# Performance work log

Measured on AMD Instinct MI355X. Metric: run time of the kernel, lower is better.

The kernel has to match this reference:

```python
import jax, jax.numpy as jnp
import numpy as np

EPS = 1e-08


def setup_inputs() -> dict:
    key = jax.random.key(0)
    kx, ky = jax.random.split(key)
    x = jax.random.normal(kx, (8192, 512), dtype=jnp.float32)
    y = jax.random.normal(ky, (8192, 512), dtype=jnp.float32)
    return {"x": x, "y": y}


def reference(x, y):
    # Faithful to torch.nn.CosineSimilarity(dim=2, eps=EPS) applied to the
    # broadcast pair (x[i], y[j]):
    #   cos[i, j] = <x_i, y_j> / (max(||x_i||, eps) * max(||y_j||, eps))
    # Algebraically equivalent efficient form: normalize rows once, then GEMM.
    xn = x / jnp.maximum(jnp.linalg.norm(x, axis=1, keepdims=True), EPS)  # [Nx, L]
    yn = y / jnp.maximum(jnp.linalg.norm(y, axis=1, keepdims=True), EPS)  # [Ny, L]
    return jnp.einsum('il,jl->ij', xn, yn)  # [Nx, Ny]
```

## Files before the change

### kernel.cpp

```cpp
#include <hip/hip_runtime.h>


typedef __attribute__((ext_vector_type(8))) short bf16x8;
typedef __attribute__((ext_vector_type(4))) float f32x4;
typedef __attribute__((ext_vector_type(8))) unsigned short ushort8;

#define M_DIM 8192
#define N_DIM 8192
#define K_DIM 512

static __device__ __forceinline__ unsigned short f32_to_bf16(float f) {
  unsigned int u = __float_as_uint(f);
  u = (u + 0x7FFFu + ((u >> 16) & 1u)) >> 16;
  return (unsigned short)u;
}

__global__ __launch_bounds__(256) void normalize_rows(
    const float* __restrict__ x, const float* __restrict__ y,
    unsigned short* __restrict__ out) {
  const int wid = threadIdx.x >> 6;
  const int lane = threadIdx.x & 63;
  const int row = (blockIdx.x << 2) + wid;
  const float* src = row < M_DIM ? x + (size_t)row * K_DIM
                                 : y + (size_t)(row - M_DIM) * K_DIM;
  const float4* r = (const float4*)src;
  float4 v0 = r[lane * 2];
  float4 v1 = r[lane * 2 + 1];
  float ss = v0.x * v0.x + v0.y * v0.y + v0.z * v0.z + v0.w * v0.w +
             v1.x * v1.x + v1.y * v1.y + v1.z * v1.z + v1.w * v1.w;
#pragma unroll
  for (int off = 32; off; off >>= 1) ss += __shfl_xor(ss, off, 64);
  const float s = 1.0f / fmaxf(sqrtf(ss), 1e-8f);
  const float f[8] = {v0.x, v0.y, v0.z, v0.w, v1.x, v1.y, v1.z, v1.w};
  union { ushort8 v; unsigned short u[8]; } o;
#pragma unroll
  for (int i = 0; i < 8; ++i) o.u[i] = f32_to_bf16(f[i] * s);
  *(ushort8*)(out + (size_t)row * K_DIM + lane * 8) = o.v;
}

static __device__ __forceinline__ void gl16(const unsigned short* g, char* l) {
  __builtin_amdgcn_global_load_lds(
      (const __attribute__((address_space(1))) unsigned int*)g,
      (__attribute__((address_space(3))) unsigned int*)l, 16, 0, 0);
}

#define BAR() __builtin_amdgcn_s_barrier()
#define SBAR() __builtin_amdgcn_sched_barrier(0)
#define LGKM0() do { asm volatile("s_waitcnt lgkmcnt(0)" ::: "memory"); \
                     __builtin_amdgcn_sched_barrier(0); } while (0)
#define VMCNT(n) do { asm volatile("s_waitcnt vmcnt(" #n ")" ::: "memory"); \
                      __builtin_amdgcn_sched_barrier(0); } while (0)

__global__ __launch_bounds__(256, 3) void cosgemm(
    const unsigned short* __restrict__ A,
    const unsigned short* __restrict__ B,
    float* __restrict__ C) {
  extern __shared__ char smem[];

  const int tid = threadIdx.x;
  const int lane = tid & 63;
  const int wid = tid >> 6;
  const int wm = wid >> 1;
  const int wn = wid & 1;
  const int lr16 = lane & 15;
  const int hq = lane >> 4;
  const int sw = hq ^ (lr16 & 3);

  const int bid = blockIdx.x;
  const int idx = bid >> 3;
  const int by = ((bid & 7) << 3) + (idx & 7);
  const int bx = idx >> 3;
  const int row0 = by << 7;
  const int col0 = bx << 7;

  const int srl = lane >> 2;
  const int ssl = (lane & 3) ^ (srl & 3);
  const unsigned short* pA =
      A + (size_t)(row0 + (wid << 4) + srl) * K_DIM + ssl * 8;
  const unsigned short* pB =
      B + (size_t)(col0 + (wid << 4) + srl) * K_DIM + ssl * 8;

  auto stageA = [&](int buf, int h, int T) {
    char* l = smem + buf * 16384 + (h << 12) + (wid << 10);
    gl16(pA + T * 32 + (size_t)(h << 6) * K_DIM, l);
  };
  auto stageB = [&](int buf, int h, int T) {
    char* l = smem + buf * 16384 + 8192 + (h << 12) + (wid << 10);
    gl16(pB + T * 32 + (size_t)(h << 6) * K_DIM, l);
  };

  bf16x8 af[4], bf[4];
  f32x4 acc[4][4] = {};

  auto ldA = [&](int buf) {
#pragma unroll
    for (int m = 0; m < 4; ++m) {
      const int row = (wm << 6) + m * 16 + lr16;
      af[m] = *(const bf16x8*)(smem + buf * 16384 + row * 64 + (sw << 4));
    }
  };
  auto ldB = [&](int buf, int g) {
#pragma unroll
    for (int j = 0; j < 2; ++j) {
      const int row = (wn << 6) + (g * 2 + j) * 16 + lr16;
      bf[g * 2 + j] = *(const bf16x8*)(smem + buf * 16384 + 8192 + row * 64 +
                                       (sw << 4));
    }
  };
  auto mm = [&](int g) {
    __builtin_amdgcn_s_setprio(1);
#pragma unroll
    for (int m = 0; m < 4; ++m)
#pragma unroll
      for (int j = 0; j < 2; ++j)
        acc[m][g * 2 + j] = __builtin_amdgcn_mfma_f32_16x16x32_bf16(
            af[m], bf[g * 2 + j], acc[m][g * 2 + j], 0, 0, 0);
    __builtin_amdgcn_s_setprio(0);
  };

  stageA(0, 0, 0); stageA(0, 1, 0); stageB(0, 0, 0); stageB(0, 1, 0);
  stageA(1, 0, 1); stageA(1, 1, 1); stageB(1, 0, 1); stageB(1, 1, 1);
  VMCNT(4);
  BAR(); SBAR();

#pragma unroll 1
  for (int t = 0; t < 16; ++t) {
    const int cb = t % 3, nb = (t + 2) % 3;
    const bool st = (t < 14);
    ldA(cb); ldB(cb, 0);
    if (st) { stageA(nb, 0, t + 2); stageA(nb, 1, t + 2); }
    BAR(); LGKM0(); mm(0); BAR();
    ldB(cb, 1);
    if (st) { stageB(nb, 0, t + 2); stageB(nb, 1, t + 2); }
    BAR(); LGKM0(); mm(1);
    if (st) { VMCNT(4); } else { VMCNT(0); }
    BAR(); SBAR();
  }

  float* S = (float*)(smem + wid * 4352);
  const int crow0 = row0 + (wm << 6);
  const int ccol0 = col0 + (wn << 6);
#pragma unroll
  for (int fm = 0; fm < 4; ++fm) {
#pragma unroll
    for (int fn = 0; fn < 4; ++fn)
#pragma unroll
      for (int q = 0; q < 4; ++q)
        S[(hq * 4 + q) * 68 + fn * 16 + lr16] = acc[fm][fn][q];
#pragma unroll
    for (int r = 0; r < 4; ++r) {
      f32x4 v = *(const f32x4*)&S[(r * 4 + hq) * 68 + lr16 * 4];
      __builtin_nontemporal_store(
          v, (f32x4*)&C[(size_t)(crow0 + fm * 16 + r * 4 + hq) * N_DIM +
                        ccol0 + lr16 * 4]);
    }
  }
}

extern "C" void kernel_launch(void* const* d_in, const int* in_sizes, int n_in,
                              void* d_out, int out_size, void* d_ws, size_t ws_size,
                              hipStream_t stream) {
  const float* x = (const float*)d_in[0];
  const float* y = (const float*)d_in[1];
  float* out = (float*)d_out;
  unsigned short* xn = (unsigned short*)d_ws;
  unsigned short* yn = xn + (size_t)M_DIM * K_DIM;

  (void)hipFuncSetAttribute((const void*)cosgemm,
                            hipFuncAttributeMaxDynamicSharedMemorySize, 49152);

  normalize_rows<<<(M_DIM + N_DIM) / 4, 256, 0, stream>>>(x, y, xn);
  cosgemm<<<(M_DIM / 128) * (N_DIM / 128), 256, 49152, stream>>>(xn, yn, out);
}
```

Measured before the change: 111.1 us.

## Give each wave private LDS tiles and drop block barriers in GEMM loop

```diff
diff --git a/kernel.cpp b/kernel.cpp
--- a/kernel.cpp
+++ b/kernel.cpp
@@ -44,14 +44,13 @@
       (__attribute__((address_space(3))) unsigned int*)l, 16, 0, 0);
 }
 
-#define BAR() __builtin_amdgcn_s_barrier()
 #define SBAR() __builtin_amdgcn_sched_barrier(0)
 #define LGKM0() do { asm volatile("s_waitcnt lgkmcnt(0)" ::: "memory"); \
                      __builtin_amdgcn_sched_barrier(0); } while (0)
 #define VMCNT(n) do { asm volatile("s_waitcnt vmcnt(" #n ")" ::: "memory"); \
                       __builtin_amdgcn_sched_barrier(0); } while (0)
 
-__global__ __launch_bounds__(256, 3) void cosgemm(
+__global__ __launch_bounds__(256, 2) void cosgemm(
     const unsigned short* __restrict__ A,
     const unsigned short* __restrict__ B,
     float* __restrict__ C) {
@@ -70,76 +69,64 @@
   const int idx = bid >> 3;
   const int by = ((bid & 7) << 3) + (idx & 7);
   const int bx = idx >> 3;
-  const int row0 = by << 7;
-  const int col0 = bx << 7;
+  const int row0 = (by << 7) + (wm << 6);
+  const int col0 = (bx << 7) + (wn << 6);
 
   const int srl = lane >> 2;
   const int ssl = (lane & 3) ^ (srl & 3);
-  const unsigned short* pA =
-      A + (size_t)(row0 + (wid << 4) + srl) * K_DIM + ssl * 8;
-  const unsigned short* pB =
-      B + (size_t)(col0 + (wid << 4) + srl) * K_DIM + ssl * 8;
+  const unsigned short* pA = A + (size_t)(row0 + srl) * K_DIM + ssl * 8;
+  const unsigned short* pB = B + (size_t)(col0 + srl) * K_DIM + ssl * 8;
+  char* const myLds = smem + (wid << 14);
 
-  auto stageA = [&](int buf, int h, int T) {
-    char* l = smem + buf * 16384 + (h << 12) + (wid << 10);
-    gl16(pA + T * 32 + (size_t)(h << 6) * K_DIM, l);
-  };
-  auto stageB = [&](int buf, int h, int T) {
-    char* l = smem + buf * 16384 + 8192 + (h << 12) + (wid << 10);
-    gl16(pB + T * 32 + (size_t)(h << 6) * K_DIM, l);
+  auto stage = [&](int par, int T) {
+    char* l = myLds + (par << 13);
+#pragma unroll
+    for (int c = 0; c < 4; ++c) {
+      gl16(pA + T * 32 + (size_t)(c << 4) * K_DIM, l + (c << 10));
+      gl16(pB + T * 32 + (size_t)(c << 4) * K_DIM, l + 4096 + (c << 10));
+    }
   };
 
   bf16x8 af[4], bf[4];
   f32x4 acc[4][4] = {};
 
-  auto ldA = [&](int buf) {
+  auto ldAB = [&](int par) {
 #pragma unroll
-    for (int m = 0; m < 4; ++m) {
-      const int row = (wm << 6) + m * 16 + lr16;
-      af[m] = *(const bf16x8*)(smem + buf * 16384 + row * 64 + (sw << 4));
-    }
+    for (int m = 0; m < 4; ++m)
+      af[m] = *(const bf16x8*)(myLds + (par << 13) + (m * 16 + lr16) * 64 +
+                               (sw << 4));
+#pragma unroll
+    for (int n = 0; n < 4; ++n)
+      bf[n] = *(const bf16x8*)(myLds + (par << 13) + 4096 +
+                               (n * 16 + lr16) * 64 + (sw << 4));
   };
-  auto ldB = [&](int buf, int g) {
-#pragma unroll
-    for (int j = 0; j < 2; ++j) {
-      const int row = (wn << 6) + (g * 2 + j) * 16 + lr16;
-      bf[g * 2 + j] = *(const bf16x8*)(smem + buf * 16384 + 8192 + row * 64 +
-                                       (sw << 4));
-    }
-  };
-  auto mm = [&](int g) {
+  auto mmAll = [&]() {
     __builtin_amdgcn_s_setprio(1);
 #pragma unroll
     for (int m = 0; m < 4; ++m)
 #pragma unroll
-      for (int j = 0; j < 2; ++j)
-        acc[m][g * 2 + j] = __builtin_amdgcn_mfma_f32_16x16x32_bf16(
-            af[m], bf[g * 2 + j], acc[m][g * 2 + j], 0, 0, 0);
+      for (int n = 0; n < 4; ++n)
+        acc[m][n] = __builtin_amdgcn_mfma_f32_16x16x32_bf16(af[m], bf[n],
+                                                            acc[m][n], 0, 0, 0);
     __builtin_amdgcn_s_setprio(0);
   };
 
-  stageA(0, 0, 0); stageA(0, 1, 0); stageB(0, 0, 0); stageB(0, 1, 0);
-  stageA(1, 0, 1); stageA(1, 1, 1); stageB(1, 0, 1); stageB(1, 1, 1);
-  VMCNT(4);
-  BAR(); SBAR();
+  stage(0, 0);
+  stage(1, 1);
+  VMCNT(8);
 
 #pragma unroll 1
   for (int t = 0; t < 16; ++t) {
-    const int cb = t % 3, nb = (t + 2) % 3;
-    const bool st = (t < 14);
-    ldA(cb); ldB(cb, 0);
-    if (st) { stageA(nb, 0, t + 2); stageA(nb, 1, t + 2); }
-    BAR(); LGKM0(); mm(0); BAR();
-    ldB(cb, 1);
-    if (st) { stageB(nb, 0, t + 2); stageB(nb, 1, t + 2); }
-    BAR(); LGKM0(); mm(1);
-    if (st) { VMCNT(4); } else { VMCNT(0); }
-    BAR(); SBAR();
+    const int cb = t & 1;
+    ldAB(cb);
+    LGKM0();
+    if (t < 14) stage(cb, t + 2);
+    mmAll();
+    if (t < 14) { VMCNT(8); }
+    else if (t == 14) { VMCNT(0); }
   }
 
-  float* S = (float*)(smem + wid * 4352);
-  const int crow0 = row0 + (wm << 6);
-  const int ccol0 = col0 + (wn << 6);
+  float* S = (float*)myLds;
 #pragma unroll
   for (int fm = 0; fm < 4; ++fm) {
 #pragma unroll
@@ -147,13 +134,15 @@
 #pragma unroll
       for (int q = 0; q < 4; ++q)
         S[(hq * 4 + q) * 68 + fn * 16 + lr16] = acc[fm][fn][q];
+    LGKM0();
 #pragma unroll
     for (int r = 0; r < 4; ++r) {
       f32x4 v = *(const f32x4*)&S[(r * 4 + hq) * 68 + lr16 * 4];
       __builtin_nontemporal_store(
-          v, (f32x4*)&C[(size_t)(crow0 + fm * 16 + r * 4 + hq) * N_DIM +
-                        ccol0 + lr16 * 4]);
+          v, (f32x4*)&C[(size_t)(row0 + fm * 16 + r * 4 + hq) * N_DIM +
+                        col0 + lr16 * 4]);
     }
+    LGKM0();
   }
 }
 
@@ -167,8 +156,8 @@
   unsigned short* yn = xn + (size_t)M_DIM * K_DIM;
 
   (void)hipFuncSetAttribute((const void*)cosgemm,
-                            hipFuncAttributeMaxDynamicSharedMemorySize, 49152);
+                            hipFuncAttributeMaxDynamicSharedMemorySize, 65536);
 
   normalize_rows<<<(M_DIM + N_DIM) / 4, 256, 0, stream>>>(x, y, xn);
-  cosgemm<<<(M_DIM / 128) * (N_DIM / 128), 256, 49152, stream>>>(xn, yn, out);
+  cosgemm<<<(M_DIM / 128) * (N_DIM / 128), 256, 65536, stream>>>(xn, yn, out);
 }
```

New measurement: 134.5 us. 1.21x slower.
